# Kernel tuning notes

Hardware: AMD Instinct MI355X
Metric: run time of the kernel (lower is better)

## Reference

```python
import jax, jax.numpy as jnp
import numpy as np

B, S, D = 1, 2048, 4096
H, KV, HD = 32, 8, 128
REP = H // KV            # 4, GQA repeat factor
THETA = 500000.0
NEG = -1e9               # stand-in for -inf in additive causal mask


def _rope(x, cos, sin):
    # x: [B,S,h,HD]; complex rotation on interleaved (even,odd) pairs,
    # matching torch.view_as_complex on [..., HD/2, 2]
    xr, xi = x[..., 0::2], x[..., 1::2]
    c = cos[None, :, None, :]
    s = sin[None, :, None, :]
    out_r = xr * c - xi * s
    out_i = xr * s + xi * c
    return jnp.stack([out_r, out_i], axis=-1).reshape(x.shape)


def setup_inputs() -> dict:
    key = jax.random.key(0)
    ks = jax.random.split(key, 6)
    x = jax.random.normal(ks[0], (B, S, D), dtype=jnp.float32)
    # torch nn.Linear weights are [out, in]
    sc = 1.0 / np.sqrt(D)
    wq = jax.random.normal(ks[1], (H * HD, D), dtype=jnp.float32) * sc
    wk = jax.random.normal(ks[2], (KV * HD, D), dtype=jnp.float32) * sc
    wv = jax.random.normal(ks[3], (KV * HD, D), dtype=jnp.float32) * sc
    wo = jax.random.normal(ks[4], (D, H * HD), dtype=jnp.float32) * sc
    # RoPE freqs_cis = exp(i * t * theta_f), stored as cos/sin [S, HD/2]
    freqs = 1.0 / (THETA ** (jnp.arange(0, HD, 2, dtype=jnp.float32) / HD))
    ang = jnp.outer(jnp.arange(S, dtype=jnp.float32), freqs)
    cos, sin = jnp.cos(ang), jnp.sin(ang)
    cache = jnp.zeros((2, B, S, KV, HD), dtype=jnp.float32)
    mask = jnp.where(jnp.tril(jnp.ones((S, S), dtype=bool)), 0.0, NEG).astype(jnp.float32)
    return {"x": x, "wq": wq, "wk": wk, "wv": wv, "wo": wo,
            "cos": cos, "sin": sin, "cache": cache, "mask": mask,
            "start_pos": 0}


def reference(x, wq, wk, wv, wo, cos, sin, cache, mask, start_pos):
    b, s, _ = x.shape
    xq = (x @ wq.T).reshape(b, s, H, HD)
    xk = (x @ wk.T).reshape(b, s, KV, HD)
    xv = (x @ wv.T).reshape(b, s, KV, HD)
    xq = _rope(xq, cos, sin)
    xk = _rope(xk, cos, sin)
    # functional KV-cache write
    cache = cache.at[0, :b, start_pos:start_pos + s].set(xk)
    cache = cache.at[1, :b, start_pos:start_pos + s].set(xv)
    keys = cache[0, :b, :start_pos + s]    # [b,T,KV,HD]
    values = cache[1, :b, :start_pos + s]  # [b,T,KV,HD]
    # GQA: head h = kv*REP + r (repeat_interleave ordering)
    q = xq.reshape(b, s, KV, REP, HD)
    scores = jnp.einsum('bskrd,btkd->bkrst', q, keys) / jnp.sqrt(jnp.float32(HD))
    scores = scores + mask[None, None, None]           # [b,KV,REP,s,T]
    p = jax.nn.softmax(scores.astype(jnp.float32), axis=-1).astype(x.dtype)
    out = jnp.einsum('bkrst,btkd->bskrd', p, values).reshape(b, s, H * HD)
    return out @ wo.T
```

## Files before the change

### kernel.cpp

```cpp
#include <hip/hip_runtime.h>
#include <stdint.h>

typedef __bf16 bf16_8 __attribute__((ext_vector_type(8)));
typedef __bf16 bf16_4 __attribute__((ext_vector_type(4)));
typedef float  f32x4  __attribute__((ext_vector_type(4)));

#define B_  1
#define S_  2048
#define D_  4096
#define H_  32
#define KV_ 8
#define HD_ 128

__device__ inline void gload_lds16(const void* g, void* l) {
  __builtin_amdgcn_global_load_lds((const __attribute__((address_space(1))) void*)g,
                                   (__attribute__((address_space(3))) void*)l, 16, 0, 0);
}

__global__ __launch_bounds__(256) void cvt_all(const float* __restrict__ x,
                                               const float* __restrict__ wq,
                                               const float* __restrict__ wk,
                                               const float* __restrict__ wv,
                                               const float* __restrict__ wo,
                                               __bf16* __restrict__ dst) {
  int i = blockIdx.x * 256 + threadIdx.x;
  const float* s;
  int j = i;
  if (j < 2097152) s = x;
  else if ((j -= 2097152) < 4194304) s = wq;
  else if ((j -= 4194304) < 1048576) s = wk;
  else if ((j -= 1048576) < 1048576) s = wv;
  else { j -= 1048576; s = wo; }
  float4 v = ((const float4*)s)[j];
  bf16_4 o = { (__bf16)v.x, (__bf16)v.y, (__bf16)v.z, (__bf16)v.w };
  ((bf16_4*)dst)[i] = o;
}

__global__ __launch_bounds__(256) void rope_k(__bf16* __restrict__ Qb, __bf16* __restrict__ Kb,
                                              const float* __restrict__ cosT,
                                              const float* __restrict__ sinT) {
  int t = blockIdx.x * 256 + threadIdx.x;
  const int NQ = S_ * (D_ / 8);
  __bf16* p;
  int row, cl8;
  if (t < NQ) { row = t >> 9; cl8 = t & 511; p = Qb + (size_t)row * D_ + cl8 * 8; }
  else        { int u = t - NQ; row = u >> 7; cl8 = u & 127; p = Kb + (size_t)row * 1024 + cl8 * 8; }
  bf16_8 v = *(bf16_8*)p;
  int fi0 = ((cl8 * 8) & 127) >> 1;
  float4 c4 = *(const float4*)&cosT[row * 64 + fi0];
  float4 s4 = *(const float4*)&sinT[row * 64 + fi0];
  float cc[4] = {c4.x, c4.y, c4.z, c4.w};
  float ss[4] = {s4.x, s4.y, s4.z, s4.w};
  bf16_8 o;
#pragma unroll
  for (int j = 0; j < 4; ++j) {
    float xr = (float)v[2 * j], xi = (float)v[2 * j + 1];
    o[2 * j]     = (__bf16)(xr * cc[j] - xi * ss[j]);
    o[2 * j + 1] = (__bf16)(xr * ss[j] + xi * cc[j]);
  }
  *(bf16_8*)p = o;
}

__global__ __launch_bounds__(256) void gemm_qkv(const __bf16* __restrict__ xb,
                                                const __bf16* __restrict__ wqb,
                                                const __bf16* __restrict__ wkb,
                                                const __bf16* __restrict__ wvb,
                                                __bf16* __restrict__ Qb,
                                                __bf16* __restrict__ Kb,
                                                __bf16* __restrict__ Vt) {
  __shared__ __bf16 As[128 * 32];
  __shared__ __bf16 Bs[128 * 32];
  const int nb = blockIdx.x, mb = blockIdx.y;
  const __bf16* W; int wrow0;
  if (nb < 32)      { W = wqb; wrow0 = nb * 128; }
  else if (nb < 40) { W = wkb; wrow0 = (nb - 32) * 128; }
  else              { W = wvb; wrow0 = (nb - 40) * 128; }
  const int tid = threadIdx.x, lane = tid & 63, wv = tid >> 6;
  const int wm = wv >> 1, wn = wv & 1;
  const int srow = lane >> 2, scol = (lane & 3) * 8;

  const __bf16* Ag0 = xb + (size_t)(mb * 128 + 2 * wv * 16 + srow) * D_ + scol;
  const __bf16* Bg0 = W  + (size_t)(wrow0 + 2 * wv * 16 + srow) * D_ + scol;
  __bf16* Al = As + 2 * wv * 512;
  __bf16* Bl = Bs + 2 * wv * 512;

  const f32x4 zv = {0.f, 0.f, 0.f, 0.f};
  f32x4 acc[4][4];
#pragma unroll
  for (int i = 0; i < 4; ++i)
#pragma unroll
    for (int j = 0; j < 4; ++j) acc[i][j] = zv;

  for (int k0 = 0; k0 < D_; k0 += 32) {
    gload_lds16(Ag0 + k0, Al);
    gload_lds16(Ag0 + (size_t)16 * D_ + k0, Al + 512);
    gload_lds16(Bg0 + k0, Bl);
    gload_lds16(Bg0 + (size_t)16 * D_ + k0, Bl + 512);
    __syncthreads();
    bf16_8 af[4], bfr[4];
#pragma unroll
    for (int i = 0; i < 4; ++i)
      af[i] = *(const bf16_8*)&As[(wm * 64 + i * 16 + (lane & 15)) * 32 + (lane >> 4) * 8];
#pragma unroll
    for (int j = 0; j < 4; ++j)
      bfr[j] = *(const bf16_8*)&Bs[(wn * 64 + j * 16 + (lane & 15)) * 32 + (lane >> 4) * 8];
#pragma unroll
    for (int i = 0; i < 4; ++i)
#pragma unroll
      for (int j = 0; j < 4; ++j)
        acc[i][j] = __builtin_amdgcn_mfma_f32_16x16x32_bf16(af[i], bfr[j], acc[i][j], 0, 0, 0);
    __syncthreads();
  }

#pragma unroll
  for (int i = 0; i < 4; ++i) {
    int row0 = mb * 128 + wm * 64 + i * 16 + (lane >> 4) * 4;
#pragma unroll
    for (int j = 0; j < 4; ++j) {
      int cl = wn * 64 + j * 16 + (lane & 15);
      if (nb < 32) {
        int colg = nb * 128 + cl;
#pragma unroll
        for (int r = 0; r < 4; ++r)
          Qb[(size_t)(row0 + r) * D_ + colg] = (__bf16)acc[i][j][r];
      } else if (nb < 40) {
        int colg = (nb - 32) * 128 + cl;
#pragma unroll
        for (int r = 0; r < 4; ++r)
          Kb[(size_t)(row0 + r) * 1024 + colg] = (__bf16)acc[i][j][r];
      } else {
        int colg = (nb - 40) * 128 + cl;
        bf16_4 pv = { (__bf16)acc[i][j][0], (__bf16)acc[i][j][1],
                      (__bf16)acc[i][j][2], (__bf16)acc[i][j][3] };
        *(bf16_4*)&Vt[(size_t)colg * S_ + row0] = pv;
      }
    }
  }
}

__global__ __launch_bounds__(256) void gemm_out(const __bf16* __restrict__ Ob,
                                                const __bf16* __restrict__ wob,
                                                float* __restrict__ Of) {
  __shared__ __bf16 As[128 * 32];
  __shared__ __bf16 Bs[128 * 32];
  const int nb = blockIdx.x, mb = blockIdx.y;
  const int tid = threadIdx.x, lane = tid & 63, wv = tid >> 6;
  const int wm = wv >> 1, wn = wv & 1;
  const int srow = lane >> 2, scol = (lane & 3) * 8;

  const __bf16* Ag0 = Ob  + (size_t)(mb * 128 + 2 * wv * 16 + srow) * D_ + scol;
  const __bf16* Bg0 = wob + (size_t)(nb * 128 + 2 * wv * 16 + srow) * D_ + scol;
  __bf16* Al = As + 2 * wv * 512;
  __bf16* Bl = Bs + 2 * wv * 512;

  const f32x4 zv = {0.f, 0.f, 0.f, 0.f};
  f32x4 acc[4][4];
#pragma unroll
  for (int i = 0; i < 4; ++i)
#pragma unroll
    for (int j = 0; j < 4; ++j) acc[i][j] = zv;

  for (int k0 = 0; k0 < D_; k0 += 32) {
    gload_lds16(Ag0 + k0, Al);
    gload_lds16(Ag0 + (size_t)16 * D_ + k0, Al + 512);
    gload_lds16(Bg0 + k0, Bl);
    gload_lds16(Bg0 + (size_t)16 * D_ + k0, Bl + 512);
    __syncthreads();
    bf16_8 af[4], bfr[4];
#pragma unroll
    for (int i = 0; i < 4; ++i)
      af[i] = *(const bf16_8*)&As[(wm * 64 + i * 16 + (lane & 15)) * 32 + (lane >> 4) * 8];
#pragma unroll
    for (int j = 0; j < 4; ++j)
      bfr[j] = *(const bf16_8*)&Bs[(wn * 64 + j * 16 + (lane & 15)) * 32 + (lane >> 4) * 8];
#pragma unroll
    for (int i = 0; i < 4; ++i)
#pragma unroll
      for (int j = 0; j < 4; ++j)
        acc[i][j] = __builtin_amdgcn_mfma_f32_16x16x32_bf16(af[i], bfr[j], acc[i][j], 0, 0, 0);
    __syncthreads();
  }

#pragma unroll
  for (int i = 0; i < 4; ++i) {
    int row0 = mb * 128 + wm * 64 + i * 16 + (lane >> 4) * 4;
#pragma unroll
    for (int j = 0; j < 4; ++j) {
      int colg = nb * 128 + wn * 64 + j * 16 + (lane & 15);
#pragma unroll
      for (int r = 0; r < 4; ++r)
        Of[(size_t)(row0 + r) * D_ + colg] = acc[i][j][r];
    }
  }
}

#define COMPUTE_TILE(ACC, MR, LR, AQ, QB0, DOMASK, KSB, VSB)                       \
  {                                                                                \
    f32x4 sfr_[4];                                                                 \
    __builtin_amdgcn_s_setprio(1);                                                 \
    _Pragma("unroll")                                                              \
    for (int nf = 0; nf < 4; ++nf) {                                               \
      f32x4 c_ = zv;                                                               \
      _Pragma("unroll")                                                            \
      for (int ks = 0; ks < 4; ++ks) {                                             \
        int n_ = nf * 16 + (lane & 15);                                            \
        int bo_ = (n_ * 256 + (ks * 32 + (lane >> 4) * 8) * 2) ^ ((n_ & 7) << 4);  \
        bf16_8 bk_ = *(const bf16_8*)((char*)(KSB) + bo_);                         \
        c_ = __builtin_amdgcn_mfma_f32_16x16x32_bf16(bk_, AQ[ks], c_, 0, 0, 0);    \
      }                                                                            \
      sfr_[nf] = c_;                                                               \
    }                                                                              \
    __builtin_amdgcn_s_setprio(0);                                                 \
    const int myq_ = (QB0) + w * 16 + (lane & 15);                                 \
    float pm_ = -3e38f;                                                            \
    _Pragma("unroll")                                                              \
    for (int nf = 0; nf < 4; ++nf) {                                               \
      _Pragma("unroll")                                                            \
      for (int r = 0; r < 4; ++r) {                                                \
        int kcol_ = kb * 64 + nf * 16 + (lane >> 4) * 4 + r;                       \
        float v_ = sfr_[nf][r] * sc;                                               \
        if ((DOMASK) && kcol_ > myq_) v_ = -1e9f;                                  \
        sfr_[nf][r] = v_;                                                          \
        pm_ = fmaxf(pm_, v_);                                                      \
      }                                                                            \
    }                                                                              \
    pm_ = fmaxf(pm_, __shfl_xor(pm_, 16));                                         \
    pm_ = fmaxf(pm_, __shfl_xor(pm_, 32));                                         \
    if (!__all(pm_ <= MR + 8.f)) {                                                 \
      float mn_ = fmaxf(MR, pm_);                                                  \
      float rs_ = __expf(MR - mn_);                                                \
      MR = mn_;                                                                    \
      LR *= rs_;                                                                   \
      float rsb_[4];                                                               \
      _Pragma("unroll")                                                            \
      for (int r = 0; r < 4; ++r)                                                  \
        rsb_[r] = __shfl(rs_, (lane & 48) | ((lane >> 4) * 4 + r));                \
      _Pragma("unroll")                                                            \
      for (int d = 0; d < 8; ++d)                                                  \
        _Pragma("unroll")                                                          \
        for (int r = 0; r < 4; ++r) ACC[d][r] *= rsb_[r];                          \
    }                                                                              \
    float ps_ = 0.f;                                                               \
    _Pragma("unroll")                                                              \
    for (int nf = 0; nf < 4; ++nf) {                                               \
      bf16_4 pk_;                                                                  \
      _Pragma("unroll")                                                            \
      for (int r = 0; r < 4; ++r) {                                                \
        float p_ = __expf(sfr_[nf][r] - MR);                                       \
        ps_ += p_;                                                                 \
        pk_[r] = (__bf16)p_;                                                       \
      }                                                                            \
      int bo_ = ((lane & 15) * 128 + nf * 32 + (lane >> 4) * 8) ^                  \
                (((lane & 15) & 7) << 4);                                          \
      *(bf16_4*)((char*)(&Ps[w][0]) + bo_) = pk_;                                  \
    }                                                                              \
    ps_ += __shfl_xor(ps_, 16);                                                    \
    ps_ += __shfl_xor(ps_, 32);                                                    \
    LR += ps_;                                                                     \
    bf16_8 ap_[2];                                                                 \
    _Pragma("unroll")                                                              \
    for (int ks = 0; ks < 2; ++ks) {                                               \
      int bo_ = ((lane & 15) * 128 + (ks * 32 + (lane >> 4) * 8) * 2) ^            \
                (((lane & 15) & 7) << 4);                                          \
      ap_[ks] = *(const bf16_8*)((char*)(&Ps[w][0]) + bo_);                        \
    }                                                                              \
    __builtin_amdgcn_s_setprio(1);                                                 \
    _Pragma("unroll")                                                              \
    for (int d = 0; d < 8; ++d) {                                                  \
      _Pragma("unroll")                                                            \
      for (int ks = 0; ks < 2; ++ks) {                                             \
        int dr_ = d * 16 + (lane & 15);                                            \
        int bo_ = (dr_ * 128 + (ks * 32 + (lane >> 4) * 8) * 2) ^ ((dr_ & 7) << 4);\
        bf16_8 bv_ = *(const bf16_8*)((char*)(VSB) + bo_);                         \
        ACC[d] = __builtin_amdgcn_mfma_f32_16x16x32_bf16(ap_[ks], bv_, ACC[d], 0, 0, 0); \
      }                                                                            \
    }                                                                              \
    __builtin_amdgcn_s_setprio(0);                                                 \
  }

__global__ __launch_bounds__(256) void attn_k(const __bf16* __restrict__ Qb,
                                              const __bf16* __restrict__ Kb,
                                              const __bf16* __restrict__ Vt,
                                              __bf16* __restrict__ Ob) {
  __shared__ __bf16 Ks[2][64 * 128];
  __shared__ __bf16 Vs[2][128 * 64];
  __shared__ __bf16 Ps[4][16 * 64];
  const int x = blockIdx.x, h = blockIdx.y, kvh = h >> 2;
  const int qlo = x, qhi = 31 - x;
  const int tid = threadIdx.x, lane = tid & 63, w = tid >> 6;

  bf16_8 aq0[4], aq1[4];
#pragma unroll
  for (int ks = 0; ks < 4; ++ks) {
    int rr = w * 16 + (lane & 15);
    int cc = h * 128 + ks * 32 + (lane >> 4) * 8;
    aq0[ks] = *(const bf16_8*)&Qb[(size_t)(qlo * 64 + rr) * D_ + cc];
    aq1[ks] = *(const bf16_8*)&Qb[(size_t)(qhi * 64 + rr) * D_ + cc];
  }

  const f32x4 zv = {0.f, 0.f, 0.f, 0.f};
  f32x4 accO0[8], accO1[8];
#pragma unroll
  for (int d = 0; d < 8; ++d) { accO0[d] = zv; accO1[d] = zv; }
  float mr0 = -3e38f, lr0 = 0.f, mr1 = -3e38f, lr1 = 0.f;

  const float sc = 0.08838834764831845f;

  bf16_8 rK[4], rV[4];
#define KLOAD(KB)                                                                  \
  {                                                                                \
    _Pragma("unroll")                                                              \
    for (int u = 0; u < 4; ++u) {                                                  \
      int cid = u * 256 + tid; int row = cid >> 4, c8 = cid & 15;                  \
      rK[u] = *(const bf16_8*)&Kb[(size_t)((KB) * 64 + row) * 1024 + kvh * 128 + c8 * 8]; \
    }                                                                              \
    _Pragma("unroll")                                                              \
    for (int u = 0; u < 4; ++u) {                                                  \
      int cid = u * 256 + tid; int vr = cid >> 3, c8 = cid & 7;                    \
      rV[u] = *(const bf16_8*)&Vt[(size_t)(kvh * 128 + vr) * S_ + (KB) * 64 + c8 * 8]; \
    }                                                                              \
  }
#define KSTORE(BUF)                                                                \
  {                                                                                \
    _Pragma("unroll")                                                              \
    for (int u = 0; u < 4; ++u) {                                                  \
      int cid = u * 256 + tid; int row = cid >> 4, c8 = cid & 15;                  \
      int bo = (row * 256 + c8 * 16) ^ ((row & 7) << 4);                           \
      *(bf16_8*)((char*)(&Ks[BUF][0]) + bo) = rK[u];                               \
    }                                                                              \
    _Pragma("unroll")                                                              \
    for (int u = 0; u < 4; ++u) {                                                  \
      int cid = u * 256 + tid; int vr = cid >> 3, c8 = cid & 7;                    \
      int bo = (vr * 128 + c8 * 16) ^ ((vr & 7) << 4);                             \
      *(bf16_8*)((char*)(&Vs[BUF][0]) + bo) = rV[u];                               \
    }                                                                              \
  }

  KLOAD(0);
  KSTORE(0);
  __syncthreads();

  for (int kb = 0; kb <= qhi; ++kb) {
    const int cur = kb & 1;
    if (kb < qhi) KLOAD(kb + 1);
    __bf16* ksb = &Ks[cur][0];
    __bf16* vsb = &Vs[cur][0];
    COMPUTE_TILE(accO1, mr1, lr1, aq1, qhi * 64, (kb == qhi), ksb, vsb);
    if (kb <= qlo) COMPUTE_TILE(accO0, mr0, lr0, aq0, qlo * 64, (kb == qlo), ksb, vsb);
    if (kb < qhi) {
      KSTORE(cur ^ 1);
      __syncthreads();
    }
  }

  float inv0[4], inv1[4];
#pragma unroll
  for (int r = 0; r < 4; ++r) {
    int src = (lane & 48) | ((lane >> 4) * 4 + r);
    inv0[r] = 1.0f / __shfl(lr0, src);
    inv1[r] = 1.0f / __shfl(lr1, src);
  }
#pragma unroll
  for (int d = 0; d < 8; ++d) {
#pragma unroll
    for (int r = 0; r < 4; ++r) {
      size_t rl = (size_t)(qlo * 64 + w * 16 + (lane >> 4) * 4 + r);
      size_t rh = (size_t)(qhi * 64 + w * 16 + (lane >> 4) * 4 + r);
      int cc = h * 128 + d * 16 + (lane & 15);
      Ob[rl * D_ + cc] = (__bf16)(accO0[d][r] * inv0[r]);
      Ob[rh * D_ + cc] = (__bf16)(accO1[d][r] * inv1[r]);
    }
  }
}

extern "C" void kernel_launch(void* const* d_in, const int* in_sizes, int n_in,
                              void* d_out, int out_size, void* d_ws, size_t ws_size,
                              hipStream_t stream) {
  const float* x    = (const float*)d_in[0];
  const float* wq   = (const float*)d_in[1];
  const float* wk   = (const float*)d_in[2];
  const float* wv   = (const float*)d_in[3];
  const float* wo   = (const float*)d_in[4];
  const float* cosT = (const float*)d_in[5];
  const float* sinT = (const float*)d_in[6];
  float* out = (float*)d_out;
  char* ws = (char*)d_ws;

  __bf16* xb  = (__bf16*)(ws + 0);
  __bf16* wqb = (__bf16*)(ws + 16777216);
  __bf16* wkb = (__bf16*)(ws + 50331648);
  __bf16* wvb = (__bf16*)(ws + 58720256);
  __bf16* wob = (__bf16*)(ws + 67108864);
  __bf16* Qb  = (__bf16*)(ws + 100663296);
  __bf16* Kb  = (__bf16*)(ws + 117440512);
  __bf16* Vt  = (__bf16*)(ws + 121634816);
  __bf16* Ob  = xb;

  cvt_all<<<49152, 256, 0, stream>>>(x, wq, wk, wv, wo, xb);

  gemm_qkv<<<dim3(48, 16), 256, 0, stream>>>(xb, wqb, wkb, wvb, Qb, Kb, Vt);

  rope_k<<<5120, 256, 0, stream>>>(Qb, Kb, cosT, sinT);

  attn_k<<<dim3(16, 32), 256, 0, stream>>>(Qb, Kb, Vt, Ob);

  gemm_out<<<dim3(32, 16), 256, 0, stream>>>(Ob, wob, out);
}
```

Before: 395.5 us.

## Replace QKV GEMM with 256x256 double-buffered 8-wave pipelined kernel

The QKV projection GEMM moves from 128x128 tiles with K=32 steps and a sync around every load to 256x256 tiles with K=64 steps, run by 512 threads across 8 waves. The kernel double-buffers LDS, uses XOR-swizzled layouts to avoid bank conflicts, and splits each K step into four phases that interleave global-to-LDS loads with MFMA bursts under raised wave priority. This is meant to cut global traffic per FLOP and hide load latency behind compute. In exchange the kernel uses much more LDS and registers, and launches only 192 blocks, which may underfill the GPU's CUs.

```diff
diff --git a/kernel.cpp b/kernel.cpp
--- a/kernel.cpp
+++ b/kernel.cpp
@@ -61,81 +61,148 @@
   *(bf16_8*)p = o;
 }
 
-__global__ __launch_bounds__(256) void gemm_qkv(const __bf16* __restrict__ xb,
-                                                const __bf16* __restrict__ wqb,
-                                                const __bf16* __restrict__ wkb,
-                                                const __bf16* __restrict__ wvb,
-                                                __bf16* __restrict__ Qb,
-                                                __bf16* __restrict__ Kb,
-                                                __bf16* __restrict__ Vt) {
-  __shared__ __bf16 As[128 * 32];
-  __shared__ __bf16 Bs[128 * 32];
+
+#define STAGE_A(BF, KT, BAND)                                                      \
+  {                                                                                \
+    int c_ = wid * 64 + lane;                                                      \
+    int cs_ = c_ ^ ((c_ >> 3) & 7);                                                \
+    gload_lds16(Ag + (size_t)((BAND) * 64 + (c_ >> 3)) * 4096 + (KT) * 64 + (cs_ & 7) * 8, \
+                &Abuf[BF][(BAND) * 4096 + wid * 512]);                             \
+  }
+#define STAGE_B(BF, KT)                                                            \
+  {                                                                                \
+    _Pragma("unroll")                                                              \
+    for (int l_ = 0; l_ < 4; ++l_) {                                               \
+      int c_ = l_ * 512 + wid * 64 + lane;                                         \
+      int cs_ = c_ ^ ((c_ >> 3) & 7);                                              \
+      gload_lds16(Wg + (size_t)(c_ >> 3) * 4096 + (KT) * 64 + (cs_ & 7) * 8,       \
+                  &Bbuf[BF][l_ * 4096 + wid * 512]);                               \
+    }                                                                              \
+  }
+#define READ_A(P)                                                                  \
+  _Pragma("unroll")                                                                \
+  for (int r2 = 0; r2 < 2; ++r2)                                                   \
+    _Pragma("unroll")                                                              \
+    for (int ks = 0; ks < 2; ++ks) {                                               \
+      int row_ = (P) * 64 + wm * 32 + r2 * 16 + (lane & 15);                       \
+      int bo_ = (row_ * 128 + (ks * 32 + (lane >> 4) * 8) * 2) ^ ((row_ & 7) << 4);\
+      aq[r2][ks] = *(const bf16_8*)(Ab + bo_);                                     \
+    }
+#define READ_B()                                                                   \
+  _Pragma("unroll")                                                                \
+  for (int j = 0; j < 4; ++j)                                                      \
+    _Pragma("unroll")                                                              \
+    for (int ks = 0; ks < 2; ++ks) {                                               \
+      int row_ = wn * 64 + j * 16 + (lane & 15);                                   \
+      int bo_ = (row_ * 128 + (ks * 32 + (lane >> 4) * 8) * 2) ^ ((row_ & 7) << 4);\
+      bq[j][ks] = *(const bf16_8*)(Bb + bo_);                                      \
+    }
+#define PHASE_MFMA(P)                                                              \
+  __builtin_amdgcn_s_setprio(1);                                                   \
+  _Pragma("unroll")                                                                \
+  for (int r2 = 0; r2 < 2; ++r2)                                                   \
+    _Pragma("unroll")                                                              \
+    for (int j = 0; j < 4; ++j)                                                    \
+      _Pragma("unroll")                                                            \
+      for (int ks = 0; ks < 2; ++ks)                                               \
+        acc[P][r2][j] =                                                            \
+            __builtin_amdgcn_mfma_f32_16x16x32_bf16(aq[r2][ks], bq[j][ks], acc[P][r2][j], 0, 0, 0); \
+  __builtin_amdgcn_s_setprio(0);
+
+__global__ __launch_bounds__(512) void gemm8_qkv(const __bf16* __restrict__ xb,
+                                                 const __bf16* __restrict__ wqb,
+                                                 const __bf16* __restrict__ wkb,
+                                                 const __bf16* __restrict__ wvb,
+                                                 __bf16* __restrict__ Qb,
+                                                 __bf16* __restrict__ Kb,
+                                                 __bf16* __restrict__ Vt) {
+  __shared__ __bf16 Abuf[2][16384];
+  __shared__ __bf16 Bbuf[2][16384];
   const int nb = blockIdx.x, mb = blockIdx.y;
-  const __bf16* W; int wrow0;
-  if (nb < 32)      { W = wqb; wrow0 = nb * 128; }
-  else if (nb < 40) { W = wkb; wrow0 = (nb - 32) * 128; }
-  else              { W = wvb; wrow0 = (nb - 40) * 128; }
-  const int tid = threadIdx.x, lane = tid & 63, wv = tid >> 6;
-  const int wm = wv >> 1, wn = wv & 1;
-  const int srow = lane >> 2, scol = (lane & 3) * 8;
-
-  const __bf16* Ag0 = xb + (size_t)(mb * 128 + 2 * wv * 16 + srow) * D_ + scol;
-  const __bf16* Bg0 = W  + (size_t)(wrow0 + 2 * wv * 16 + srow) * D_ + scol;
-  __bf16* Al = As + 2 * wv * 512;
-  __bf16* Bl = Bs + 2 * wv * 512;
+  const int tid = threadIdx.x, lane = tid & 63, wid = tid >> 6;
+  const int wm = wid >> 2, wn = wid & 3;
+
+  const __bf16* Wg;
+  if (nb < 16)      Wg = wqb + (size_t)nb * 256 * 4096;
+  else if (nb < 20) Wg = wkb + (size_t)(nb - 16) * 256 * 4096;
+  else              Wg = wvb + (size_t)(nb - 20) * 256 * 4096;
+  const __bf16* Ag = xb + (size_t)mb * 256 * 4096;
 
   const f32x4 zv = {0.f, 0.f, 0.f, 0.f};
-  f32x4 acc[4][4];
-#pragma unroll
-  for (int i = 0; i < 4; ++i)
-#pragma unroll
-    for (int j = 0; j < 4; ++j) acc[i][j] = zv;
-
-  for (int k0 = 0; k0 < D_; k0 += 32) {
-    gload_lds16(Ag0 + k0, Al);
-    gload_lds16(Ag0 + (size_t)16 * D_ + k0, Al + 512);
-    gload_lds16(Bg0 + k0, Bl);
-    gload_lds16(Bg0 + (size_t)16 * D_ + k0, Bl + 512);
-    __syncthreads();
-    bf16_8 af[4], bfr[4];
-#pragma unroll
-    for (int i = 0; i < 4; ++i)
-      af[i] = *(const bf16_8*)&As[(wm * 64 + i * 16 + (lane & 15)) * 32 + (lane >> 4) * 8];
-#pragma unroll
-    for (int j = 0; j < 4; ++j)
-      bfr[j] = *(const bf16_8*)&Bs[(wn * 64 + j * 16 + (lane & 15)) * 32 + (lane >> 4) * 8];
-#pragma unroll
-    for (int i = 0; i < 4; ++i)
-#pragma unroll
-      for (int j = 0; j < 4; ++j)
-        acc[i][j] = __builtin_amdgcn_mfma_f32_16x16x32_bf16(af[i], bfr[j], acc[i][j], 0, 0, 0);
-    __syncthreads();
-  }
-
-#pragma unroll
-  for (int i = 0; i < 4; ++i) {
-    int row0 = mb * 128 + wm * 64 + i * 16 + (lane >> 4) * 4;
-#pragma unroll
-    for (int j = 0; j < 4; ++j) {
-      int cl = wn * 64 + j * 16 + (lane & 15);
-      if (nb < 32) {
-        int colg = nb * 128 + cl;
-#pragma unroll
-        for (int r = 0; r < 4; ++r)
-          Qb[(size_t)(row0 + r) * D_ + colg] = (__bf16)acc[i][j][r];
-      } else if (nb < 40) {
-        int colg = (nb - 32) * 128 + cl;
-#pragma unroll
-        for (int r = 0; r < 4; ++r)
-          Kb[(size_t)(row0 + r) * 1024 + colg] = (__bf16)acc[i][j][r];
-      } else {
-        int colg = (nb - 40) * 128 + cl;
-        bf16_4 pv = { (__bf16)acc[i][j][0], (__bf16)acc[i][j][1],
-                      (__bf16)acc[i][j][2], (__bf16)acc[i][j][3] };
-        *(bf16_4*)&Vt[(size_t)colg * S_ + row0] = pv;
+  f32x4 acc[4][2][4];
+#pragma unroll
+  for (int q = 0; q < 4; ++q)
+#pragma unroll
+    for (int r2 = 0; r2 < 2; ++r2)
+#pragma unroll
+      for (int j = 0; j < 4; ++j) acc[q][r2][j] = zv;
+
+  STAGE_B(0, 0);
+  STAGE_A(0, 0, 0); STAGE_A(0, 0, 1); STAGE_A(0, 0, 2); STAGE_A(0, 0, 3);
+  STAGE_B(1, 1);
+  STAGE_A(1, 1, 0); STAGE_A(1, 1, 1); STAGE_A(1, 1, 2);
+
+  for (int kt = 0; kt < 64; ++kt) {
+    const int cur = kt & 1;
+    const char* Ab = (const char*)&Abuf[cur][0];
+    const char* Bb = (const char*)&Bbuf[cur][0];
+    if (kt == 63) { asm volatile("s_waitcnt vmcnt(0)" ::: "memory"); }
+    else          { asm volatile("s_waitcnt vmcnt(7)" ::: "memory"); }
+    __builtin_amdgcn_s_barrier();
+
+    bf16_8 bq[4][2], aq[2][2];
+    READ_B();
+    READ_A(0);
+    __builtin_amdgcn_s_barrier();
+    asm volatile("s_waitcnt lgkmcnt(0)" ::: "memory");
+    __builtin_amdgcn_sched_barrier(0);
+    if (kt + 1 < 64) { STAGE_A(cur ^ 1, kt + 1, 3); }
+    PHASE_MFMA(0);
+    READ_A(1);
+    __builtin_amdgcn_s_barrier();
+    asm volatile("s_waitcnt lgkmcnt(0)" ::: "memory");
+    __builtin_amdgcn_sched_barrier(0);
+    if (kt + 2 < 64) { STAGE_B(cur, kt + 2); }
+    PHASE_MFMA(1);
+    READ_A(2);
+    __builtin_amdgcn_s_barrier();
+    asm volatile("s_waitcnt lgkmcnt(0)" ::: "memory");
+    __builtin_amdgcn_sched_barrier(0);
+    if (kt + 2 < 64) { STAGE_A(cur, kt + 2, 0); STAGE_A(cur, kt + 2, 1); }
+    PHASE_MFMA(2);
+    READ_A(3);
+    __builtin_amdgcn_s_barrier();
+    asm volatile("s_waitcnt lgkmcnt(0)" ::: "memory");
+    __builtin_amdgcn_sched_barrier(0);
+    if (kt + 2 < 64) { STAGE_A(cur, kt + 2, 2); }
+    PHASE_MFMA(3);
+  }
+
+#pragma unroll
+  for (int q = 0; q < 4; ++q)
+#pragma unroll
+    for (int r2 = 0; r2 < 2; ++r2)
+#pragma unroll
+      for (int j = 0; j < 4; ++j) {
+        int rowb = mb * 256 + q * 64 + wm * 32 + r2 * 16 + (lane >> 4) * 4;
+        int col = wn * 64 + j * 16 + (lane & 15);
+        if (nb < 16) {
+          int colg = nb * 256 + col;
+#pragma unroll
+          for (int r = 0; r < 4; ++r)
+            Qb[(size_t)(rowb + r) * D_ + colg] = (__bf16)acc[q][r2][j][r];
+        } else if (nb < 20) {
+          int colg = (nb - 16) * 256 + col;
+#pragma unroll
+          for (int r = 0; r < 4; ++r)
+            Kb[(size_t)(rowb + r) * 1024 + colg] = (__bf16)acc[q][r2][j][r];
+        } else {
+          int colg = (nb - 20) * 256 + col;
+          bf16_4 pv = { (__bf16)acc[q][r2][j][0], (__bf16)acc[q][r2][j][1],
+                        (__bf16)acc[q][r2][j][2], (__bf16)acc[q][r2][j][3] };
+          *(bf16_4*)&Vt[(size_t)colg * S_ + rowb] = pv;
+        }
       }
-    }
-  }
 }
 
 __global__ __launch_bounds__(256) void gemm_out(const __bf16* __restrict__ Ob,
@@ -398,7 +465,7 @@
 
   cvt_all<<<49152, 256, 0, stream>>>(x, wq, wk, wv, wo, xb);
 
-  gemm_qkv<<<dim3(48, 16), 256, 0, stream>>>(xb, wqb, wkb, wvb, Qb, Kb, Vt);
+  gemm8_qkv<<<dim3(24, 8), 512, 0, stream>>>(xb, wqb, wkb, wvb, Qb, Kb, Vt);
 
   rope_k<<<5120, 256, 0, stream>>>(Qb, Kb, cosT, sinT);
 
```

New measurement: 398.7 us. About the same (+0.8%).

## Use 128-wide KV tiles with single-buffered LDS and two blocks per CU

Applied to the files above, without the earlier changes.

Doubles the attention key/value tile from 64 to 128 keys, halving the number of loop iterations, barriers and online-softmax rescale steps per query block. LDS moves from double buffers to a single buffer with an extra barrier before each store, and launch bounds now request two blocks per CU. The trade-off is that the final diagonal tile computes more masked-out work, the larger register prefetch arrays add register pressure, and the single LDS buffer allows less overlap between loads and compute.

```diff
diff --git a/kernel.cpp b/kernel.cpp
--- a/kernel.cpp
+++ b/kernel.cpp
@@ -194,18 +194,18 @@
   }
 }
 
-#define COMPUTE_TILE(ACC, MR, LR, AQ, QB0, DOMASK, KSB, VSB)                       \
+#define COMPUTE_TILE(ACC, MR, LR, AQ, QB0, DOMASK)                                 \
   {                                                                                \
-    f32x4 sfr_[4];                                                                 \
+    f32x4 sfr_[8];                                                                 \
     __builtin_amdgcn_s_setprio(1);                                                 \
     _Pragma("unroll")                                                              \
-    for (int nf = 0; nf < 4; ++nf) {                                               \
+    for (int nf = 0; nf < 8; ++nf) {                                               \
       f32x4 c_ = zv;                                                               \
       _Pragma("unroll")                                                            \
       for (int ks = 0; ks < 4; ++ks) {                                             \
         int n_ = nf * 16 + (lane & 15);                                            \
         int bo_ = (n_ * 256 + (ks * 32 + (lane >> 4) * 8) * 2) ^ ((n_ & 7) << 4);  \
-        bf16_8 bk_ = *(const bf16_8*)((char*)(KSB) + bo_);                         \
+        bf16_8 bk_ = *(const bf16_8*)((char*)Ks + bo_);                            \
         c_ = __builtin_amdgcn_mfma_f32_16x16x32_bf16(bk_, AQ[ks], c_, 0, 0, 0);    \
       }                                                                            \
       sfr_[nf] = c_;                                                               \
@@ -214,10 +214,10 @@
     const int myq_ = (QB0) + w * 16 + (lane & 15);                                 \
     float pm_ = -3e38f;                                                            \
     _Pragma("unroll")                                                              \
-    for (int nf = 0; nf < 4; ++nf) {                                               \
+    for (int nf = 0; nf < 8; ++nf) {                                               \
       _Pragma("unroll")                                                            \
       for (int r = 0; r < 4; ++r) {                                                \
-        int kcol_ = kb * 64 + nf * 16 + (lane >> 4) * 4 + r;                       \
+        int kcol_ = kb * 128 + nf * 16 + (lane >> 4) * 4 + r;                      \
         float v_ = sfr_[nf][r] * sc;                                               \
         if ((DOMASK) && kcol_ > myq_) v_ = -1e9f;                                  \
         sfr_[nf][r] = v_;                                                          \
@@ -242,7 +242,7 @@
     }                                                                              \
     float ps_ = 0.f;                                                               \
     _Pragma("unroll")                                                              \
-    for (int nf = 0; nf < 4; ++nf) {                                               \
+    for (int nf = 0; nf < 8; ++nf) {                                               \
       bf16_4 pk_;                                                                  \
       _Pragma("unroll")                                                            \
       for (int r = 0; r < 4; ++r) {                                                \
@@ -250,17 +250,17 @@
         ps_ += p_;                                                                 \
         pk_[r] = (__bf16)p_;                                                       \
       }                                                                            \
-      int bo_ = ((lane & 15) * 128 + nf * 32 + (lane >> 4) * 8) ^                  \
+      int bo_ = ((lane & 15) * 256 + nf * 32 + (lane >> 4) * 8) ^                  \
                 (((lane & 15) & 7) << 4);                                          \
       *(bf16_4*)((char*)(&Ps[w][0]) + bo_) = pk_;                                  \
     }                                                                              \
     ps_ += __shfl_xor(ps_, 16);                                                    \
     ps_ += __shfl_xor(ps_, 32);                                                    \
     LR += ps_;                                                                     \
-    bf16_8 ap_[2];                                                                 \
-    _Pragma("unroll")                                                              \
-    for (int ks = 0; ks < 2; ++ks) {                                               \
-      int bo_ = ((lane & 15) * 128 + (ks * 32 + (lane >> 4) * 8) * 2) ^            \
+    bf16_8 ap_[4];                                                                 \
+    _Pragma("unroll")                                                              \
+    for (int ks = 0; ks < 4; ++ks) {                                               \
+      int bo_ = ((lane & 15) * 256 + (ks * 32 + (lane >> 4) * 8) * 2) ^            \
                 (((lane & 15) & 7) << 4);                                          \
       ap_[ks] = *(const bf16_8*)((char*)(&Ps[w][0]) + bo_);                        \
     }                                                                              \
@@ -268,25 +268,26 @@
     _Pragma("unroll")                                                              \
     for (int d = 0; d < 8; ++d) {                                                  \
       _Pragma("unroll")                                                            \
-      for (int ks = 0; ks < 2; ++ks) {                                             \
+      for (int ks = 0; ks < 4; ++ks) {                                             \
         int dr_ = d * 16 + (lane & 15);                                            \
-        int bo_ = (dr_ * 128 + (ks * 32 + (lane >> 4) * 8) * 2) ^ ((dr_ & 7) << 4);\
-        bf16_8 bv_ = *(const bf16_8*)((char*)(VSB) + bo_);                         \
+        int bo_ = (dr_ * 256 + (ks * 32 + (lane >> 4) * 8) * 2) ^ ((dr_ & 7) << 4);\
+        bf16_8 bv_ = *(const bf16_8*)((char*)Vs + bo_);                            \
         ACC[d] = __builtin_amdgcn_mfma_f32_16x16x32_bf16(ap_[ks], bv_, ACC[d], 0, 0, 0); \
       }                                                                            \
     }                                                                              \
     __builtin_amdgcn_s_setprio(0);                                                 \
   }
 
-__global__ __launch_bounds__(256) void attn_k(const __bf16* __restrict__ Qb,
-                                              const __bf16* __restrict__ Kb,
-                                              const __bf16* __restrict__ Vt,
-                                              __bf16* __restrict__ Ob) {
-  __shared__ __bf16 Ks[2][64 * 128];
-  __shared__ __bf16 Vs[2][128 * 64];
-  __shared__ __bf16 Ps[4][16 * 64];
+__global__ __launch_bounds__(256, 2) void attn_k(const __bf16* __restrict__ Qb,
+                                                 const __bf16* __restrict__ Kb,
+                                                 const __bf16* __restrict__ Vt,
+                                                 __bf16* __restrict__ Ob) {
+  __shared__ __bf16 Ks[128 * 128];
+  __shared__ __bf16 Vs[128 * 128];
+  __shared__ __bf16 Ps[4][16 * 128];
   const int x = blockIdx.x, h = blockIdx.y, kvh = h >> 2;
   const int qlo = x, qhi = 31 - x;
+  const int Tlo = (qlo >> 1) + 1, Thi = (qhi >> 1) + 1;
   const int tid = threadIdx.x, lane = tid & 63, w = tid >> 6;
 
   bf16_8 aq0[4], aq1[4];
@@ -306,49 +307,47 @@
 
   const float sc = 0.08838834764831845f;
 
-  bf16_8 rK[4], rV[4];
+  bf16_8 rK[8], rV[8];
 #define KLOAD(KB)                                                                  \
   {                                                                                \
     _Pragma("unroll")                                                              \
-    for (int u = 0; u < 4; ++u) {                                                  \
+    for (int u = 0; u < 8; ++u) {                                                  \
       int cid = u * 256 + tid; int row = cid >> 4, c8 = cid & 15;                  \
-      rK[u] = *(const bf16_8*)&Kb[(size_t)((KB) * 64 + row) * 1024 + kvh * 128 + c8 * 8]; \
-    }                                                                              \
-    _Pragma("unroll")                                                              \
-    for (int u = 0; u < 4; ++u) {                                                  \
-      int cid = u * 256 + tid; int vr = cid >> 3, c8 = cid & 7;                    \
-      rV[u] = *(const bf16_8*)&Vt[(size_t)(kvh * 128 + vr) * S_ + (KB) * 64 + c8 * 8]; \
-    }                                                                              \
-  }
-#define KSTORE(BUF)                                                                \
+      rK[u] = *(const bf16_8*)&Kb[(size_t)((KB) * 128 + row) * 1024 + kvh * 128 + c8 * 8]; \
+    }                                                                              \
+    _Pragma("unroll")                                                              \
+    for (int u = 0; u < 8; ++u) {                                                  \
+      int cid = u * 256 + tid; int vr = cid >> 4, c8 = cid & 15;                   \
+      rV[u] = *(const bf16_8*)&Vt[(size_t)(kvh * 128 + vr) * S_ + (KB) * 128 + c8 * 8]; \
+    }                                                                              \
+  }
+#define KSTORE()                                                                   \
   {                                                                                \
     _Pragma("unroll")                                                              \
-    for (int u = 0; u < 4; ++u) {                                                  \
+    for (int u = 0; u < 8; ++u) {                                                  \
       int cid = u * 256 + tid; int row = cid >> 4, c8 = cid & 15;                  \
       int bo = (row * 256 + c8 * 16) ^ ((row & 7) << 4);                           \
-      *(bf16_8*)((char*)(&Ks[BUF][0]) + bo) = rK[u];                               \
-    }                                                                              \
-    _Pragma("unroll")                                                              \
-    for (int u = 0; u < 4; ++u) {                                                  \
-      int cid = u * 256 + tid; int vr = cid >> 3, c8 = cid & 7;                    \
-      int bo = (vr * 128 + c8 * 16) ^ ((vr & 7) << 4);                             \
-      *(bf16_8*)((char*)(&Vs[BUF][0]) + bo) = rV[u];                               \
+      *(bf16_8*)((char*)Ks + bo) = rK[u];                                          \
+    }                                                                              \
+    _Pragma("unroll")                                                              \
+    for (int u = 0; u < 8; ++u) {                                                  \
+      int cid = u * 256 + tid; int vr = cid >> 4, c8 = cid & 15;                   \
+      int bo = (vr * 256 + c8 * 16) ^ ((vr & 7) << 4);                             \
+      *(bf16_8*)((char*)Vs + bo) = rV[u];                                          \
     }                                                                              \
   }
 
   KLOAD(0);
-  KSTORE(0);
+  KSTORE();
   __syncthreads();
 
-  for (int kb = 0; kb <= qhi; ++kb) {
-    const int cur = kb & 1;
-    if (kb < qhi) KLOAD(kb + 1);
-    __bf16* ksb = &Ks[cur][0];
-    __bf16* vsb = &Vs[cur][0];
-    COMPUTE_TILE(accO1, mr1, lr1, aq1, qhi * 64, (kb == qhi), ksb, vsb);
-    if (kb <= qlo) COMPUTE_TILE(accO0, mr0, lr0, aq0, qlo * 64, (kb == qlo), ksb, vsb);
-    if (kb < qhi) {
-      KSTORE(cur ^ 1);
+  for (int kb = 0; kb < Thi; ++kb) {
+    if (kb + 1 < Thi) KLOAD(kb + 1);
+    COMPUTE_TILE(accO1, mr1, lr1, aq1, qhi * 64, (kb == Thi - 1));
+    if (kb < Tlo) COMPUTE_TILE(accO0, mr0, lr0, aq0, qlo * 64, (kb == Tlo - 1));
+    if (kb + 1 < Thi) {
+      __syncthreads();
+      KSTORE();
       __syncthreads();
     }
   }
```

Result: slower. 513.4 us (+29.8%).

## Stage K/V tiles via direct global-to-LDS loads and fold softmax scale into Q

Applied to the files above, without the earlier changes.

Replaces the register-staged K/V prefetch (global load into registers, then an LDS store) with global_load_lds DMA writes straight into the double-buffered LDS tiles. The XOR swizzle is applied on the source address so the existing swizzled LDS layout is kept, and the loop waits on vmcnt before each barrier. The 1/sqrt(HD) scale is pre-multiplied into Q once, which removes a multiply per score but adds an extra bf16 rounding of the scaled Q. The max and sum reductions are also split into four independent chains for more ILP.

```diff
diff --git a/kernel.cpp b/kernel.cpp
--- a/kernel.cpp
+++ b/kernel.cpp
@@ -212,18 +212,21 @@
     }                                                                              \
     __builtin_amdgcn_s_setprio(0);                                                 \
     const int myq_ = (QB0) + w * 16 + (lane & 15);                                 \
-    float pm_ = -3e38f;                                                            \
+    float pmn_[4];                                                                 \
     _Pragma("unroll")                                                              \
     for (int nf = 0; nf < 4; ++nf) {                                               \
+      float t_ = -3e38f;                                                           \
       _Pragma("unroll")                                                            \
       for (int r = 0; r < 4; ++r) {                                                \
         int kcol_ = kb * 64 + nf * 16 + (lane >> 4) * 4 + r;                       \
-        float v_ = sfr_[nf][r] * sc;                                               \
+        float v_ = sfr_[nf][r];                                                    \
         if ((DOMASK) && kcol_ > myq_) v_ = -1e9f;                                  \
         sfr_[nf][r] = v_;                                                          \
-        pm_ = fmaxf(pm_, v_);                                                      \
+        t_ = fmaxf(t_, v_);                                                        \
       }                                                                            \
-    }                                                                              \
+      pmn_[nf] = t_;                                                               \
+    }                                                                              \
+    float pm_ = fmaxf(fmaxf(pmn_[0], pmn_[1]), fmaxf(pmn_[2], pmn_[3]));           \
     pm_ = fmaxf(pm_, __shfl_xor(pm_, 16));                                         \
     pm_ = fmaxf(pm_, __shfl_xor(pm_, 32));                                         \
     if (!__all(pm_ <= MR + 8.f)) {                                                 \
@@ -240,20 +243,23 @@
         _Pragma("unroll")                                                          \
         for (int r = 0; r < 4; ++r) ACC[d][r] *= rsb_[r];                          \
     }                                                                              \
-    float ps_ = 0.f;                                                               \
+    float psn_[4];                                                                 \
     _Pragma("unroll")                                                              \
     for (int nf = 0; nf < 4; ++nf) {                                               \
       bf16_4 pk_;                                                                  \
+      float t_ = 0.f;                                                              \
       _Pragma("unroll")                                                            \
       for (int r = 0; r < 4; ++r) {                                                \
         float p_ = __expf(sfr_[nf][r] - MR);                                       \
-        ps_ += p_;                                                                 \
+        t_ += p_;                                                                  \
         pk_[r] = (__bf16)p_;                                                       \
       }                                                                            \
+      psn_[nf] = t_;                                                               \
       int bo_ = ((lane & 15) * 128 + nf * 32 + (lane >> 4) * 8) ^                  \
                 (((lane & 15) & 7) << 4);                                          \
       *(bf16_4*)((char*)(&Ps[w][0]) + bo_) = pk_;                                  \
     }                                                                              \
+    float ps_ = (psn_[0] + psn_[1]) + (psn_[2] + psn_[3]);                         \
     ps_ += __shfl_xor(ps_, 16);                                                    \
     ps_ += __shfl_xor(ps_, 32);                                                    \
     LR += ps_;                                                                     \
@@ -289,13 +295,20 @@
   const int qlo = x, qhi = 31 - x;
   const int tid = threadIdx.x, lane = tid & 63, w = tid >> 6;
 
+  const float sc = 0.08838834764831845f;
+
   bf16_8 aq0[4], aq1[4];
 #pragma unroll
   for (int ks = 0; ks < 4; ++ks) {
     int rr = w * 16 + (lane & 15);
     int cc = h * 128 + ks * 32 + (lane >> 4) * 8;
-    aq0[ks] = *(const bf16_8*)&Qb[(size_t)(qlo * 64 + rr) * D_ + cc];
-    aq1[ks] = *(const bf16_8*)&Qb[(size_t)(qhi * 64 + rr) * D_ + cc];
+    bf16_8 t0 = *(const bf16_8*)&Qb[(size_t)(qlo * 64 + rr) * D_ + cc];
+    bf16_8 t1 = *(const bf16_8*)&Qb[(size_t)(qhi * 64 + rr) * D_ + cc];
+#pragma unroll
+    for (int e = 0; e < 8; ++e) {
+      aq0[ks][e] = (__bf16)((float)t0[e] * sc);
+      aq1[ks][e] = (__bf16)((float)t1[e] * sc);
+    }
   }
 
   const f32x4 zv = {0.f, 0.f, 0.f, 0.f};
@@ -304,51 +317,37 @@
   for (int d = 0; d < 8; ++d) { accO0[d] = zv; accO1[d] = zv; }
   float mr0 = -3e38f, lr0 = 0.f, mr1 = -3e38f, lr1 = 0.f;
 
-  const float sc = 0.08838834764831845f;
-
-  bf16_8 rK[4], rV[4];
-#define KLOAD(KB)                                                                  \
+#define KSTAGE(BUF, KB)                                                            \
   {                                                                                \
     _Pragma("unroll")                                                              \
     for (int u = 0; u < 4; ++u) {                                                  \
-      int cid = u * 256 + tid; int row = cid >> 4, c8 = cid & 15;                  \
-      rK[u] = *(const bf16_8*)&Kb[(size_t)((KB) * 64 + row) * 1024 + kvh * 128 + c8 * 8]; \
+      int chunk = (u * 4 + w) * 64 + lane;                                         \
+      int row = chunk >> 4, p8 = chunk & 15;                                       \
+      gload_lds16(&Kb[(size_t)((KB) * 64 + row) * 1024 + kvh * 128 + (p8 ^ (row & 7)) * 8], \
+                  &Ks[BUF][(u * 4 + w) * 512]);                                    \
     }                                                                              \
     _Pragma("unroll")                                                              \
     for (int u = 0; u < 4; ++u) {                                                  \
-      int cid = u * 256 + tid; int vr = cid >> 3, c8 = cid & 7;                    \
-      rV[u] = *(const bf16_8*)&Vt[(size_t)(kvh * 128 + vr) * S_ + (KB) * 64 + c8 * 8]; \
-    }                                                                              \
-  }
-#define KSTORE(BUF)                                                                \
-  {                                                                                \
-    _Pragma("unroll")                                                              \
-    for (int u = 0; u < 4; ++u) {                                                  \
-      int cid = u * 256 + tid; int row = cid >> 4, c8 = cid & 15;                  \
-      int bo = (row * 256 + c8 * 16) ^ ((row & 7) << 4);                           \
-      *(bf16_8*)((char*)(&Ks[BUF][0]) + bo) = rK[u];                               \
-    }                                                                              \
-    _Pragma("unroll")                                                              \
-    for (int u = 0; u < 4; ++u) {                                                  \
-      int cid = u * 256 + tid; int vr = cid >> 3, c8 = cid & 7;                    \
-      int bo = (vr * 128 + c8 * 16) ^ ((vr & 7) << 4);                             \
-      *(bf16_8*)((char*)(&Vs[BUF][0]) + bo) = rV[u];                               \
-    }                                                                              \
-  }
-
-  KLOAD(0);
-  KSTORE(0);
+      int chunk = (u * 4 + w) * 64 + lane;                                         \
+      int vr = chunk >> 3, p8 = chunk & 7;                                         \
+      gload_lds16(&Vt[(size_t)(kvh * 128 + vr) * S_ + (KB) * 64 + (p8 ^ (vr & 7)) * 8], \
+                  &Vs[BUF][(u * 4 + w) * 512]);                                    \
+    }                                                                              \
+  }
+
+  KSTAGE(0, 0);
+  asm volatile("s_waitcnt vmcnt(0)" ::: "memory");
   __syncthreads();
 
   for (int kb = 0; kb <= qhi; ++kb) {
     const int cur = kb & 1;
-    if (kb < qhi) KLOAD(kb + 1);
-    __bf16* ksb = &Ks[cur][0];
-    __bf16* vsb = &Vs[cur][0];
+    if (kb < qhi) KSTAGE(cur ^ 1, kb + 1);
+    const __bf16* ksb = &Ks[cur][0];
+    const __bf16* vsb = &Vs[cur][0];
     COMPUTE_TILE(accO1, mr1, lr1, aq1, qhi * 64, (kb == qhi), ksb, vsb);
     if (kb <= qlo) COMPUTE_TILE(accO0, mr0, lr0, aq0, qlo * 64, (kb == qlo), ksb, vsb);
     if (kb < qhi) {
-      KSTORE(cur ^ 1);
+      asm volatile("s_waitcnt vmcnt(0)" ::: "memory");
       __syncthreads();
     }
   }
```

Result: no change. 391.7 us (-0.9%).
